# Performance work log

Measured on AMD Instinct MI355X. Metric: run time of the kernel, lower is better.

Reference implementation:

```python
import jax, jax.numpy as jnp
import numpy as np

DIM = 1024
HEADS = 8
HD = DIM // HEADS          # 128
HALF = HD // 2             # 64 complex pairs
EPS = 1e-6
T, L, H, W = 10, 4, 21, 37
TOK_PER_FRAME = 1 + L * (5 + H * W)   # 3129
SK = T * TOK_PER_FRAME                # 31290
SQ = 512
THETA = 10000.0


def _inv_freqs(dim):
    # matches precompute_freqs_cis: 1/theta**(arange(0,dim,2)/dim)
    return 1.0 / THETA ** (np.arange(0, dim, 2)[: dim // 2].astype(np.float64) / dim)


def _angles(t_idx, h_idx, w_idx):
    # 3D RoPE split per precompute_freqs_cis_3d: f gets HD-2*(HD//3)=44 dims, h/w get HD//3=42 each
    hd3 = HD // 3
    inv_f = _inv_freqs(HD - 2 * hd3)  # 22 freqs
    inv_h = _inv_freqs(hd3)           # 21 freqs
    inv_w = _inv_freqs(hd3)           # 21 freqs
    ang = np.concatenate([
        t_idx[:, None] * inv_f[None, :],
        h_idx[:, None] * inv_h[None, :],
        w_idx[:, None] * inv_w[None, :],
    ], axis=-1)  # [S, 64]
    return ang


def _memory_positions():
    # per-frame layout from build_3d_freqs_unified: 1 pose token (h=w=0),
    # then per layer: 5 register tokens (h=w=0) + H*W grid tokens
    h_f, w_f = [0], [0]
    grid_h, grid_w = np.meshgrid(np.arange(H), np.arange(W), indexing='ij')
    for _ in range(L):
        h_f += [0] * 5 + list(grid_h.ravel())
        w_f += [0] * 5 + list(grid_w.ravel())
    h_f = np.asarray(h_f, np.float64)
    w_f = np.asarray(w_f, np.float64)
    t_idx = np.repeat(np.arange(T, dtype=np.float64), TOK_PER_FRAME)
    return t_idx, np.tile(h_f, T), np.tile(w_f, T)


def setup_inputs() -> dict:
    key = jax.random.key(0)
    ks = jax.random.split(key, 8)
    # RoPE angle tables
    tq = np.zeros(SQ)  # use_time_encoding=False for queries -> t=0
    hq = (np.arange(SQ) // W) % H
    wq = np.arange(SQ) % W
    ang_q = _angles(tq.astype(np.float64), hq.astype(np.float64), wq.astype(np.float64))
    tk, hk, wk = _memory_positions()
    ang_k = _angles(tk, hk, wk)
    s = 0.02
    inp = {
        'x': jax.random.normal(ks[0], (1, SQ, DIM), jnp.float32),
        'mem': jax.random.normal(ks[1], (1, SK, DIM), jnp.float32),
        'mask': jax.random.randint(ks[2], (1, SK), 0, 2) > 0,
        'cos_q': jnp.asarray(np.cos(ang_q), jnp.float32),
        'sin_q': jnp.asarray(np.sin(ang_q), jnp.float32),
        'cos_k': jnp.asarray(np.cos(ang_k), jnp.float32),
        'sin_k': jnp.asarray(np.sin(ang_k), jnp.float32),
        'Wq': jax.random.normal(ks[3], (DIM, DIM), jnp.float32) * s,
        'bq': jnp.zeros((DIM,), jnp.float32),
        'Wk': jax.random.normal(ks[4], (DIM, DIM), jnp.float32) * s,
        'bk': jnp.zeros((DIM,), jnp.float32),
        'Wv': jax.random.normal(ks[5], (DIM, DIM), jnp.float32) * s,
        'bv': jnp.zeros((DIM,), jnp.float32),
        'Wo': jax.random.normal(ks[6], (DIM, DIM), jnp.float32) * s,
        'bo': jnp.zeros((DIM,), jnp.float32),
        'gq': jnp.ones((DIM,), jnp.float32),
        'gk': jnp.ones((DIM,), jnp.float32),
    }
    return inp


def _rmsnorm(x, g):
    xf = x.astype(jnp.float32)
    y = xf * jax.lax.rsqrt(jnp.mean(xf * xf, axis=-1, keepdims=True) + EPS)
    return y.astype(x.dtype) * g


def _rope(x, cos, sin):
    # x: [B,S,D]; complex rotation on interleaved pairs per head, freqs shared across heads
    B, S, _ = x.shape
    xh = x.reshape(B, S, HEADS, HALF, 2)
    xr, xi = xh[..., 0], xh[..., 1]
    c = cos[None, :, None, :]
    s = sin[None, :, None, :]
    orr = xr * c - xi * s
    oi = xr * s + xi * c
    return jnp.stack([orr, oi], axis=-1).reshape(B, S, HEADS * HD)


def reference(x, mem, mask, cos_q, sin_q, cos_k, sin_k,
              Wq, bq, Wk, bk, Wv, bv, Wo, bo, gq, gk):
    q = _rmsnorm(x @ Wq.T + bq, gq)
    k = _rmsnorm(mem @ Wk.T + bk, gk)
    v = mem @ Wv.T + bv
    q = _rope(q, cos_q, sin_q)
    k = _rope(k, cos_k, sin_k)
    B, Sq, _ = q.shape
    Sk = k.shape[1]
    qh = q.reshape(B, Sq, HEADS, HD)
    kh = k.reshape(B, Sk, HEADS, HD)
    vh = v.reshape(B, Sk, HEADS, HD)
    scores = jnp.einsum('bqnd,bknd->bnqk', qh, kh) / jnp.sqrt(jnp.float32(HD))
    bias = jnp.where(mask[:, None, None, :], 0.0, -jnp.inf).astype(scores.dtype)
    attn = jax.nn.softmax(scores + bias, axis=-1)
    out = jnp.einsum('bnqk,bknd->bqnd', attn, vh).reshape(B, Sq, DIM)
    return out @ Wo.T + bo
```

## Files before the change

### kernel.cpp

```cpp
#include <hip/hip_runtime.h>
#include <cstdint>

typedef __bf16 bf16;
typedef __bf16 bf16x8 __attribute__((ext_vector_type(8)));
typedef __bf16 bf16x4 __attribute__((ext_vector_type(4)));
typedef float f32x4 __attribute__((ext_vector_type(4)));

#define DEVINL __device__ __forceinline__

namespace {
constexpr int DIM = 1024, HEADS = 8, HD = 128, HALF = 64;
constexpr int SQ = 512;
constexpr int SK = 31290;
constexpr int SKP = 31488;
constexpr int NSPLIT = 24;

constexpr long OFF_MEMB = 0;
constexpr long OFF_XB   = OFF_MEMB + (long)SKP * DIM * 2;
constexpr long OFF_WKV  = OFF_XB + (long)SQ * DIM * 2;
constexpr long OFF_WQ   = OFF_WKV + 2048L * DIM * 2;
constexpr long OFF_WO   = OFF_WQ + (long)DIM * DIM * 2;
constexpr long OFF_BKV  = OFF_WO + (long)DIM * DIM * 2;
constexpr long OFF_KPRE = OFF_BKV + 2048L * 4;
constexpr long OFF_VT   = OFF_KPRE + (long)SKP * DIM * 2;
constexpr long OFF_QPRE = OFF_VT + (long)DIM * SKP * 2;
constexpr long OFF_QR   = OFF_QPRE + (long)SQ * DIM * 4;
constexpr long OFF_BIAS = OFF_QR + (long)SQ * DIM * 2;
constexpr long OFF_ML   = OFF_BIAS + (long)SKP * 4;
constexpr long OFF_AO   = OFF_ML + (long)NSPLIT * HEADS * SQ * 2 * 4;
constexpr long OFF_IDX  = OFF_AO + (long)SQ * DIM * 2;
constexpr long OFF_NKC  = OFF_IDX + 31744L * 4;
constexpr long OFF_OP   = OFF_MEMB;
}

DEVINL void gl_lds16(const void* g, void* l) {
  __builtin_amdgcn_global_load_lds(
      (__attribute__((address_space(1))) void*)(void*)g,
      (__attribute__((address_space(3))) void*)l, 16, 0, 0);
}


__global__ __launch_bounds__(1024) void k_scan(const int* __restrict__ mask,
                                               int* __restrict__ idx,
                                               int* __restrict__ nkcp) {
  int tid = threadIdx.x, lane = tid & 63, wv = tid >> 6;
  __shared__ int wsum[16];
  __shared__ int base;
  if (tid == 0) base = 0;
  __syncthreads();
  for (int c = 0; c < 31; ++c) {
    int i = c * 1024 + tid;
    int m = (i < SK) ? (mask[i] != 0) : 0;
    int v = m;
    #pragma unroll
    for (int off = 1; off < 64; off <<= 1) {
      int t = __shfl_up(v, off);
      if (lane >= off) v += t;
    }
    if (lane == 63) wsum[wv] = v;
    __syncthreads();
    int woff = 0;
    for (int j = 0; j < wv; ++j) woff += wsum[j];
    if (m) idx[base + woff + v - 1] = i;
    __syncthreads();
    if (tid == 0) {
      int tot = 0;
      for (int j = 0; j < 16; ++j) tot += wsum[j];
      base += tot;
    }
    __syncthreads();
  }
  if (tid == 0) *nkcp = base;
}


__global__ __launch_bounds__(256) void k_cvt_mem(const float* __restrict__ mem,
                                                 const int* __restrict__ idx,
                                                 const int* __restrict__ nkcp,
                                                 bf16* __restrict__ memb) {
  long i = (long)blockIdx.x * 256 + threadIdx.x;
  long e = i * 8;
  if (e >= (long)SKP * DIM) return;
  int row = (int)(e >> 10);
  int nkc = *nkcp;
  int lim = ((((nkc + 63) & ~63) + 255) & ~255);
  if (row >= lim) return;
  bf16x8 o;
  if (row < nkc) {
    long se = ((long)idx[row] << 10) + (e & 1023);
    float4 a = *(const float4*)(mem + se);
    float4 b = *(const float4*)(mem + se + 4);
    o[0] = (bf16)a.x; o[1] = (bf16)a.y; o[2] = (bf16)a.z; o[3] = (bf16)a.w;
    o[4] = (bf16)b.x; o[5] = (bf16)b.y; o[6] = (bf16)b.z; o[7] = (bf16)b.w;
  } else {
    #pragma unroll
    for (int j = 0; j < 8; ++j) o[j] = (bf16)0.0f;
  }
  *(bf16x8*)(memb + e) = o;
}

__global__ __launch_bounds__(256) void k_cvt(const float* __restrict__ s,
                                             bf16* __restrict__ d, long n8) {
  long i = (long)blockIdx.x * 256 + threadIdx.x;
  if (i >= n8) return;
  long e = i * 8;
  float4 a = *(const float4*)(s + e);
  float4 b = *(const float4*)(s + e + 4);
  bf16x8 o;
  o[0] = (bf16)a.x; o[1] = (bf16)a.y; o[2] = (bf16)a.z; o[3] = (bf16)a.w;
  o[4] = (bf16)b.x; o[5] = (bf16)b.y; o[6] = (bf16)b.z; o[7] = (bf16)b.w;
  *(bf16x8*)(d + e) = o;
}

__global__ __launch_bounds__(256) void k_build_wkv(const float* __restrict__ Wk,
    const float* __restrict__ Wv, const float* __restrict__ bk,
    const float* __restrict__ bv, bf16* __restrict__ WB, float* __restrict__ bKV) {
  long i = (long)blockIdx.x * 256 + threadIdx.x;
  long e = i * 8;
  if (e < 2048L * 1024) {
    int n = (int)(e >> 10);
    const float* src = (n < 1024) ? (Wk + e) : (Wv + e - 1024L * 1024);
    float4 a = *(const float4*)(src);
    float4 b = *(const float4*)(src + 4);
    bf16x8 o;
    o[0] = (bf16)a.x; o[1] = (bf16)a.y; o[2] = (bf16)a.z; o[3] = (bf16)a.w;
    o[4] = (bf16)b.x; o[5] = (bf16)b.y; o[6] = (bf16)b.z; o[7] = (bf16)b.w;
    *(bf16x8*)(WB + e) = o;
  }
  if (i < 2048) bKV[i] = (i < 1024) ? bk[i] : bv[i - 1024];
}

__global__ __launch_bounds__(256) void k_bias(const int* __restrict__ nkcp,
                                              float* __restrict__ biasA) {
  int k = blockIdx.x * 256 + threadIdx.x;
  if (k < SKP) biasA[k] = (k < *nkcp) ? 0.0f : -1e30f;
}


template<int MODE>
__global__ __launch_bounds__(256, 2)
void k_gemm(const bf16* __restrict__ A, const bf16* __restrict__ B,
            const float* __restrict__ bias, int Mtiles, int Ntiles,
            float* __restrict__ outF, int ldF,
            bf16* __restrict__ outK, bf16* __restrict__ outVT) {
  constexpr int K = 1024;
  __shared__ char lds[32768];
  char* ldsA = lds;
  char* ldsB = lds + 16384;
  int tid = threadIdx.x;
  int w = tid >> 6, lane = tid & 63;
  int cpx = gridDim.x >> 3;
  int bid = (blockIdx.x & 7) * cpx + (blockIdx.x >> 3);
  int mt = bid / Ntiles, nt = bid % Ntiles;
  int m0 = mt * 128, n0 = nt * 128;
  int wm = w >> 1, wn = w & 1;
  int cl = lane & 15, rg = lane >> 4;

  f32x4 acc[4][4] = {};

  int rowi = lane >> 3, g = lane & 7;
  for (int kt = 0; kt < K / 64; ++kt) {
    #pragma unroll
    for (int j = 0; j < 4; ++j) {
      int rb = (w * 4 + j) * 8;
      int row = rb + rowi;
      int gs = g ^ (row & 7);
      gl_lds16((const char*)(A + (long)(m0 + row) * K + kt * 64) + gs * 16, ldsA + rb * 128);
      gl_lds16((const char*)(B + (long)(n0 + row) * K + kt * 64) + gs * 16, ldsB + rb * 128);
    }
    __syncthreads();
    #pragma unroll
    for (int ks = 0; ks < 2; ++ks) {
      bf16x8 af[4], bfr[4];
      #pragma unroll
      for (int i = 0; i < 4; ++i) {
        int rowA = wm * 64 + i * 16 + cl;
        int c = ks * 4 + rg;
        af[i] = *(const bf16x8*)(ldsA + rowA * 128 + ((c ^ (rowA & 7)) * 16));
        int rowB = wn * 64 + i * 16 + cl;
        bfr[i] = *(const bf16x8*)(ldsB + rowB * 128 + ((c ^ (rowB & 7)) * 16));
      }
      #pragma unroll
      for (int mf = 0; mf < 4; ++mf)
        #pragma unroll
        for (int nf = 0; nf < 4; ++nf)
          acc[mf][nf] = __builtin_amdgcn_mfma_f32_16x16x32_bf16(af[mf], bfr[nf], acc[mf][nf], 0, 0, 0);
    }
    __syncthreads();
  }

  #pragma unroll
  for (int mf = 0; mf < 4; ++mf) {
    #pragma unroll
    for (int nf = 0; nf < 4; ++nf) {
      int n = n0 + wn * 64 + nf * 16 + cl;
      float bval = bias[n];
      int mb = m0 + wm * 64 + mf * 16 + rg * 4;
      #pragma unroll
      for (int rr = 0; rr < 4; ++rr)
        outF[(long)(mb + rr) * ldF + n] = acc[mf][nf][rr] + bval;
    }
  }
}


#define KV_PHASE(P)                                                                   \
  {                                                                                   \
    bf16x8 a00 = dsA(cur, 2 * (P), 0),     a01 = dsA(cur, 2 * (P), 1);                \
    bf16x8 a10 = dsA(cur, 2 * (P) + 1, 0), a11 = dsA(cur, 2 * (P) + 1, 1);            \
    __builtin_amdgcn_s_setprio(1);                                                    \
    _Pragma("unroll")                                                                 \
    for (int nf = 0; nf < 4; ++nf) {                                                  \
      acc[2 * (P)][nf]     = __builtin_amdgcn_mfma_f32_16x16x32_bf16(a00, bb[nf][0], acc[2 * (P)][nf], 0, 0, 0);     \
      acc[2 * (P) + 1][nf] = __builtin_amdgcn_mfma_f32_16x16x32_bf16(a10, bb[nf][0], acc[2 * (P) + 1][nf], 0, 0, 0); \
    }                                                                                 \
    _Pragma("unroll")                                                                 \
    for (int nf = 0; nf < 4; ++nf) {                                                  \
      acc[2 * (P)][nf]     = __builtin_amdgcn_mfma_f32_16x16x32_bf16(a01, bb[nf][1], acc[2 * (P)][nf], 0, 0, 0);     \
      acc[2 * (P) + 1][nf] = __builtin_amdgcn_mfma_f32_16x16x32_bf16(a11, bb[nf][1], acc[2 * (P) + 1][nf], 0, 0, 0); \
    }                                                                                 \
    __builtin_amdgcn_s_setprio(0);                                                    \
  }

__global__ __launch_bounds__(512)
void k_gemm_kv(const bf16* __restrict__ A, const bf16* __restrict__ B,
               const float* __restrict__ bias, const int* __restrict__ nkcp,
               bf16* __restrict__ outK, bf16* __restrict__ outVT) {
  constexpr int K = 1024, NTK = 16;
  __shared__ char lds[131072];
  const int tid = threadIdx.x;
  const int w = tid >> 6, lane = tid & 63;
  const int mt = blockIdx.x >> 3, nt = blockIdx.x & 7;
  const int m0 = mt * 256, n0 = nt * 256;
  if (m0 >= ((*nkcp + 63) & ~63)) return;
  const int wm = w >> 2, wn = w & 3;
  const int cl = lane & 15, rg = lane >> 4;
  const int srow = lane >> 3, sg = lane & 7;

  f32x4 acc[8][4] = {};

  auto stage = [&](int b, int kt, int isB, int cr) {
    const bf16* src = isB ? B : A;
    int r = cr + w * 8 + srow;
    int gs = sg ^ (r & 7);
    const char* gp = (const char*)(src + (long)((isB ? n0 : m0) + r) * K + kt * 64) + gs * 16;
    char* lp = lds + b * 65536 + isB * 32768 + (cr + w * 8) * 128;
    gl_lds16(gp, lp);
  };
  auto dsA = [&](int b, int mf, int ks) -> bf16x8 {
    int r = wm * 128 + mf * 16 + cl;
    int c = ks * 4 + rg;
    return *(const bf16x8*)(lds + b * 65536 + r * 128 + ((c ^ (r & 7)) * 16));
  };
  auto dsB = [&](int b, int nf, int ks) -> bf16x8 {
    int r = wn * 64 + nf * 16 + cl;
    int c = ks * 4 + rg;
    return *(const bf16x8*)(lds + b * 65536 + 32768 + r * 128 + ((c ^ (r & 7)) * 16));
  };

  stage(0, 0, 1, 0);   stage(0, 0, 1, 64);
  stage(0, 0, 1, 128); stage(0, 0, 1, 192);
  stage(0, 0, 0, 0);   stage(0, 0, 0, 128);
  stage(0, 0, 0, 64);  stage(0, 0, 0, 192);

  for (int t = 0; t < NTK; ++t) {
    const int cur = t & 1, nxt = cur ^ 1;
    const bool pre = (t + 1 < NTK);
    bf16x8 bb[4][2];

    if (pre) {
      stage(nxt, t + 1, 1, 0); stage(nxt, t + 1, 1, 64);
      asm volatile("s_waitcnt vmcnt(4)\ns_barrier" ::: "memory");
    } else {
      asm volatile("s_waitcnt vmcnt(2)\ns_barrier" ::: "memory");
    }
    #pragma unroll
    for (int nf = 0; nf < 4; ++nf) { bb[nf][0] = dsB(cur, nf, 0); bb[nf][1] = dsB(cur, nf, 1); }
    KV_PHASE(0)
    if (pre) { stage(nxt, t + 1, 1, 128); stage(nxt, t + 1, 1, 192); }
    KV_PHASE(1)
    if (pre) {
      stage(nxt, t + 1, 0, 0); stage(nxt, t + 1, 0, 128);
      asm volatile("s_waitcnt vmcnt(6)\ns_barrier" ::: "memory");
    } else {
      asm volatile("s_waitcnt vmcnt(0)\ns_barrier" ::: "memory");
    }
    KV_PHASE(2)
    if (pre) { stage(nxt, t + 1, 0, 64); stage(nxt, t + 1, 0, 192); }
    KV_PHASE(3)
    asm volatile("s_barrier" ::: "memory");
  }

  if (nt < 4) {
    #pragma unroll
    for (int mf = 0; mf < 8; ++mf)
      #pragma unroll
      for (int nf = 0; nf < 4; ++nf) {
        int n = n0 + wn * 64 + nf * 16 + cl;
        float bval = bias[n];
        int mrow = m0 + wm * 128 + mf * 16 + rg * 4;
        #pragma unroll
        for (int rr = 0; rr < 4; ++rr)
          outK[(long)(mrow + rr) * 1024 + n] = (bf16)(acc[mf][nf][rr] + bval);
      }
  } else {
    #pragma unroll
    for (int mf = 0; mf < 8; ++mf)
      #pragma unroll
      for (int nf = 0; nf < 4; ++nf) {
        int n = n0 + wn * 64 + nf * 16 + cl;
        float bval = bias[n];
        int mrow = m0 + wm * 128 + mf * 16 + rg * 4;
        bf16x4 pk;
        #pragma unroll
        for (int rr = 0; rr < 4; ++rr) pk[rr] = (bf16)(acc[mf][nf][rr] + bval);
        *(bf16x4*)(outVT + (long)(n - 1024) * SKP + mrow) = pk;
      }
  }
}


__global__ __launch_bounds__(256) void k_fuse_q(const float* __restrict__ QP,
    bf16* __restrict__ Qr, const float* __restrict__ gg,
    const float* __restrict__ cosT, const float* __restrict__ sinT) {
  int row = blockIdx.x, tid = threadIdx.x;
  int d0 = tid * 4;
  float4 t = *(const float4*)(QP + (long)row * DIM + d0);
  float v0 = t.x, v1 = t.y, v2 = t.z, v3 = t.w;
  float ss = v0 * v0 + v1 * v1 + v2 * v2 + v3 * v3;
  #pragma unroll
  for (int m = 1; m < 64; m <<= 1) ss += __shfl_xor(ss, m);
  __shared__ float red[4];
  if ((tid & 63) == 0) red[tid >> 6] = ss;
  __syncthreads();
  float rn = rsqrtf((red[0] + red[1] + red[2] + red[3]) * (1.0f / DIM) + 1e-6f);
  v0 *= rn * gg[d0]; v1 *= rn * gg[d0 + 1]; v2 *= rn * gg[d0 + 2]; v3 *= rn * gg[d0 + 3];
  int i0 = (d0 & 127) >> 1;
  float c0 = cosT[(long)row * HALF + i0], s0 = sinT[(long)row * HALF + i0];
  float c1 = cosT[(long)row * HALF + i0 + 1], s1 = sinT[(long)row * HALF + i0 + 1];
  bf16x4 o = { (bf16)(v0 * c0 - v1 * s0), (bf16)(v0 * s0 + v1 * c0),
               (bf16)(v2 * c1 - v3 * s1), (bf16)(v2 * s1 + v3 * c1) };
  *(bf16x4*)(Qr + (long)row * DIM + d0) = o;
}

__global__ __launch_bounds__(256) void k_fuse_k(bf16* __restrict__ KP,
    const float* __restrict__ gg, const float* __restrict__ cosT,
    const float* __restrict__ sinT, const int* __restrict__ idx,
    const int* __restrict__ nkcp) {
  int row = blockIdx.x, tid = threadIdx.x;
  int nkc = *nkcp;
  if (row >= ((nkc + 63) & ~63)) return;
  int orig = (row < nkc) ? idx[row] : 0;
  int d0 = tid * 4;
  bf16x4 t = *(const bf16x4*)(KP + (long)row * DIM + d0);
  float v0 = (float)t[0], v1 = (float)t[1], v2 = (float)t[2], v3 = (float)t[3];
  float ss = v0 * v0 + v1 * v1 + v2 * v2 + v3 * v3;
  #pragma unroll
  for (int m = 1; m < 64; m <<= 1) ss += __shfl_xor(ss, m);
  __shared__ float red[4];
  if ((tid & 63) == 0) red[tid >> 6] = ss;
  __syncthreads();
  float rn = rsqrtf((red[0] + red[1] + red[2] + red[3]) * (1.0f / DIM) + 1e-6f);
  v0 *= rn * gg[d0]; v1 *= rn * gg[d0 + 1]; v2 *= rn * gg[d0 + 2]; v3 *= rn * gg[d0 + 3];
  int i0 = (d0 & 127) >> 1;
  float c0 = cosT[(long)orig * HALF + i0], s0 = sinT[(long)orig * HALF + i0];
  float c1 = cosT[(long)orig * HALF + i0 + 1], s1 = sinT[(long)orig * HALF + i0 + 1];
  bf16x4 o = { (bf16)(v0 * c0 - v1 * s0), (bf16)(v0 * s0 + v1 * c0),
               (bf16)(v2 * c1 - v3 * s1), (bf16)(v2 * s1 + v3 * c1) };
  *(bf16x4*)(KP + (long)row * DIM + d0) = o;
}


__global__ __launch_bounds__(256, 2)
void k_attn(const bf16* __restrict__ Kr, const bf16* __restrict__ VT,
            const bf16* __restrict__ Qr, const float* __restrict__ biasA,
            const int* __restrict__ nkcp,
            float* __restrict__ Opart, float* __restrict__ ml) {
  __shared__ char lds[49152];
  char* ldsK = lds;
  char* ldsV = lds + 16384;
  int tid = threadIdx.x, w = tid >> 6, lane = tid & 63;
  char* ldsP = lds + 32768 + w * 4096;
  int bid = blockIdx.x;
  int swz = (bid & 7) * 96 + (bid >> 3);
  int sp = swz >> 5, h = (swz >> 2) & 7, qb = swz & 3;
  int NTC = (*nkcp + 63) >> 6;
  int t0 = (sp * NTC) / NSPLIT;
  int t1 = ((sp + 1) * NTC) / NSPLIT;
  int cl = lane & 15, rg = lane >> 4;
  int qbase = qb * 128 + w * 32;

  bf16x8 qf[2][4];
  #pragma unroll
  for (int mf = 0; mf < 2; ++mf)
    #pragma unroll
    for (int ks = 0; ks < 4; ++ks)
      qf[mf][ks] = *(const bf16x8*)(Qr + (long)(qbase + mf * 16 + cl) * DIM + h * HD + ks * 32 + rg * 8);

  bf16x8 ones;
  #pragma unroll
  for (int j = 0; j < 8; ++j) ones[j] = (bf16)1.0f;

  f32x4 Oa[2][8] = {};
  f32x4 l_acc[2] = {};
  float m_r[2] = {-1e30f, -1e30f};

  const float sc = 0.08838834764831845f;
  for (int t = t0; t < t1; ++t) {
    int k0 = t * 64;
    __syncthreads();
    {
      int rK = lane >> 4, gK = lane & 15;
      #pragma unroll
      for (int j = 0; j < 4; ++j) {
        int rb = w * 16 + j * 4;
        int row = rb + rK;
        int gs = gK ^ (row & 7);
        gl_lds16((const char*)(Kr + (long)(k0 + row) * DIM + h * HD) + gs * 16,
                 ldsK + rb * 256);
      }
      int rV = lane >> 3, gV = lane & 7;
      #pragma unroll
      for (int j = 0; j < 4; ++j) {
        int db = w * 32 + j * 8;
        int d = db + rV;
        int gs = gV ^ (d & 7);
        gl_lds16((const char*)(VT + (long)(h * HD + d) * SKP + k0) + gs * 16,
                 ldsV + db * 128);
      }
    }
    __syncthreads();

    f32x4 sa[2][4] = {};
    #pragma unroll
    for (int ks = 0; ks < 4; ++ks) {
      #pragma unroll
      for (int nf = 0; nf < 4; ++nf) {
        int key = nf * 16 + cl;
        int c = ks * 4 + rg;
        bf16x8 kb = *(const bf16x8*)(ldsK + key * 256 + ((c ^ (key & 7)) * 16));
        sa[0][nf] = __builtin_amdgcn_mfma_f32_16x16x32_bf16(qf[0][ks], kb, sa[0][nf], 0, 0, 0);
        sa[1][nf] = __builtin_amdgcn_mfma_f32_16x16x32_bf16(qf[1][ks], kb, sa[1][nf], 0, 0, 0);
      }
    }

    float bia[4];
    #pragma unroll
    for (int nf = 0; nf < 4; ++nf) bia[nf] = biasA[k0 + nf * 16 + cl];

    #pragma unroll
    for (int mf = 0; mf < 2; ++mf) {
      char* ldsPmf = ldsP + mf * 2048;
      #pragma unroll
      for (int nf = 0; nf < 4; ++nf)
        #pragma unroll
        for (int r = 0; r < 4; ++r) sa[mf][nf][r] = sa[mf][nf][r] * sc + bia[nf];
      float mx = sa[mf][0][0];
      #pragma unroll
      for (int nf = 0; nf < 4; ++nf)
        #pragma unroll
        for (int r = 0; r < 4; ++r) mx = fmaxf(mx, sa[mf][nf][r]);
      mx = fmaxf(mx, __shfl_xor(mx, 1));
      mx = fmaxf(mx, __shfl_xor(mx, 2));
      mx = fmaxf(mx, __shfl_xor(mx, 4));
      mx = fmaxf(mx, __shfl_xor(mx, 8));
      bool grew = mx > m_r[mf] + 6.0f;
      if (__any(grew)) {
        float mn = grew ? mx : m_r[mf];
        float scale = __expf(m_r[mf] - mn);
        m_r[mf] = mn;
        l_acc[mf] *= scale;
        #pragma unroll
        for (int df = 0; df < 8; ++df) Oa[mf][df] *= scale;
      }
      #pragma unroll
      for (int nf = 0; nf < 4; ++nf)
        #pragma unroll
        for (int r = 0; r < 4; ++r) {
          float p = __expf(sa[mf][nf][r] - m_r[mf]);
          int qr = rg * 4 + r;
          int col = nf * 16 + cl;
          int gp = (col >> 3) ^ (qr & 7);
          *(bf16*)(ldsPmf + qr * 128 + gp * 16 + (col & 7) * 2) = (bf16)p;
        }
    }

    #pragma unroll
    for (int ks = 0; ks < 2; ++ks) {
      int c = ks * 4 + rg;
      bf16x8 pa0 = *(const bf16x8*)(ldsP + cl * 128 + ((c ^ (cl & 7)) * 16));
      bf16x8 pa1 = *(const bf16x8*)(ldsP + 2048 + cl * 128 + ((c ^ (cl & 7)) * 16));
      l_acc[0] = __builtin_amdgcn_mfma_f32_16x16x32_bf16(pa0, ones, l_acc[0], 0, 0, 0);
      l_acc[1] = __builtin_amdgcn_mfma_f32_16x16x32_bf16(pa1, ones, l_acc[1], 0, 0, 0);
      #pragma unroll
      for (int df = 0; df < 8; ++df) {
        int d = df * 16 + cl;
        bf16x8 vb = *(const bf16x8*)(ldsV + d * 128 + ((c ^ (d & 7)) * 16));
        Oa[0][df] = __builtin_amdgcn_mfma_f32_16x16x32_bf16(pa0, vb, Oa[0][df], 0, 0, 0);
        Oa[1][df] = __builtin_amdgcn_mfma_f32_16x16x32_bf16(pa1, vb, Oa[1][df], 0, 0, 0);
      }
    }
  }

  long rowb = (long)(sp * HEADS + h) * SQ + qbase;
  #pragma unroll
  for (int mf = 0; mf < 2; ++mf) {
    #pragma unroll
    for (int df = 0; df < 8; ++df)
      #pragma unroll
      for (int r = 0; r < 4; ++r) {
        int qr = mf * 16 + rg * 4 + r;
        Opart[(rowb + qr) * HD + df * 16 + cl] = Oa[mf][df][r];
      }
    if (cl == 0) {
      #pragma unroll
      for (int r = 0; r < 4; ++r) {
        int qr = mf * 16 + rg * 4 + r;
        ml[(rowb + qr) * 2] = m_r[mf];
        ml[(rowb + qr) * 2 + 1] = l_acc[mf][r];
      }
    }
  }
}

__global__ __launch_bounds__(128) void k_combine(const float* __restrict__ Opart,
    const float* __restrict__ ml, bf16* __restrict__ AO) {
  int bid = blockIdx.x;
  int h = bid >> 9, qq = bid & 511;
  int d = threadIdx.x;
  float M = -1e30f;
  #pragma unroll 4
  for (int s2 = 0; s2 < NSPLIT; ++s2) {
    long mi = (long)(s2 * HEADS + h) * SQ + qq;
    M = fmaxf(M, ml[mi * 2]);
  }
  float L = 0.f, acc = 0.f;
  #pragma unroll 4
  for (int s2 = 0; s2 < NSPLIT; ++s2) {
    long mi = (long)(s2 * HEADS + h) * SQ + qq;
    float wgt = __expf(ml[mi * 2] - M);
    L += wgt * ml[mi * 2 + 1];
    acc += wgt * Opart[mi * HD + d];
  }
  AO[(long)qq * DIM + h * HD + d] = (bf16)(acc / L);
}


extern "C" void kernel_launch(void* const* d_in, const int* in_sizes, int n_in,
                              void* d_out, int out_size, void* d_ws, size_t ws_size,
                              hipStream_t stream) {
  const float* x     = (const float*)d_in[0];
  const float* mem   = (const float*)d_in[1];
  const int*   mask  = (const int*)d_in[2];
  const float* cos_q = (const float*)d_in[3];
  const float* sin_q = (const float*)d_in[4];
  const float* cos_k = (const float*)d_in[5];
  const float* sin_k = (const float*)d_in[6];
  const float* Wq    = (const float*)d_in[7];
  const float* bq    = (const float*)d_in[8];
  const float* Wk    = (const float*)d_in[9];
  const float* bk    = (const float*)d_in[10];
  const float* Wv    = (const float*)d_in[11];
  const float* bv    = (const float*)d_in[12];
  const float* Wo    = (const float*)d_in[13];
  const float* bo    = (const float*)d_in[14];
  const float* gq    = (const float*)d_in[15];
  const float* gk    = (const float*)d_in[16];

  char* ws = (char*)d_ws;
  bf16*  memb = (bf16*)(ws + OFF_MEMB);
  bf16*  xb   = (bf16*)(ws + OFF_XB);
  bf16*  WkvB = (bf16*)(ws + OFF_WKV);
  bf16*  WqB  = (bf16*)(ws + OFF_WQ);
  bf16*  WoB  = (bf16*)(ws + OFF_WO);
  float* bKV  = (float*)(ws + OFF_BKV);
  bf16*  Kpre = (bf16*)(ws + OFF_KPRE);
  bf16*  VT   = (bf16*)(ws + OFF_VT);
  float* Qpre = (float*)(ws + OFF_QPRE);
  bf16*  Qr   = (bf16*)(ws + OFF_QR);
  float* biasA= (float*)(ws + OFF_BIAS);
  float* Opart= (float*)(ws + OFF_OP);
  float* mlb  = (float*)(ws + OFF_ML);
  bf16*  AO   = (bf16*)(ws + OFF_AO);
  int*   idx  = (int*)(ws + OFF_IDX);
  int*   nkcp = (int*)(ws + OFF_NKC);

  k_scan<<<dim3(1), dim3(1024), 0, stream>>>(mask, idx, nkcp);
  k_cvt_mem<<<dim3(SKP * DIM / 8 / 256), dim3(256), 0, stream>>>(mem, idx, nkcp, memb);
  k_cvt<<<dim3(SQ * DIM / 8 / 256), dim3(256), 0, stream>>>(x, xb, (long)(SQ * DIM / 8));
  k_cvt<<<dim3(DIM * DIM / 8 / 256), dim3(256), 0, stream>>>(Wq, WqB, (long)(DIM * DIM / 8));
  k_cvt<<<dim3(DIM * DIM / 8 / 256), dim3(256), 0, stream>>>(Wo, WoB, (long)(DIM * DIM / 8));
  k_build_wkv<<<dim3(2048 * DIM / 8 / 256), dim3(256), 0, stream>>>(Wk, Wv, bk, bv, WkvB, bKV);
  k_bias<<<dim3(SKP / 256), dim3(256), 0, stream>>>(nkcp, biasA);

  k_gemm<0><<<dim3(4 * 8), dim3(256), 0, stream>>>(xb, WqB, bq, 4, 8, Qpre, DIM,
                                                   (bf16*)nullptr, (bf16*)nullptr);
  k_gemm_kv<<<dim3(984), dim3(512), 0, stream>>>(memb, WkvB, bKV, nkcp, Kpre, VT);

  k_fuse_q<<<dim3(SQ), dim3(256), 0, stream>>>(Qpre, Qr, gq, cos_q, sin_q);
  k_fuse_k<<<dim3(SKP), dim3(256), 0, stream>>>(Kpre, gk, cos_k, sin_k, idx, nkcp);

  k_attn<<<dim3(NSPLIT * HEADS * 4), dim3(256), 0, stream>>>(Kpre, VT, Qr, biasA, nkcp, Opart, mlb);
  k_combine<<<dim3(HEADS * SQ), dim3(128), 0, stream>>>(Opart, mlb, AO);

  k_gemm<0><<<dim3(4 * 8), dim3(256), 0, stream>>>(AO, WoB, bo, 4, 8, (float*)d_out, DIM,
                                                   (bf16*)nullptr, (bf16*)nullptr);
  (void)in_sizes; (void)n_in; (void)out_size; (void)ws_size;
}
```

Measured before the change: 278.9 us.

## Merge conversion kernels, fuse bias fill, ballot-based scan, add KV gemm barriers

Replaces the shuffle-based prefix scan with a ballot/popcount compaction and folds the attention bias fill into the memory conversion kernel. The separate x, Wq, Wo and Wk/Wv conversion launches are merged into a single prep kernel to cut launch overhead. Extra workgroup barriers are inserted between phases of the KV GEMM main loop, likely to guard LDS buffer reuse, at the cost of more synchronization.

```diff
diff --git a/kernel.cpp b/kernel.cpp
--- a/kernel.cpp
+++ b/kernel.cpp
@@ -51,20 +51,18 @@
   for (int c = 0; c < 31; ++c) {
     int i = c * 1024 + tid;
     int m = (i < SK) ? (mask[i] != 0) : 0;
-    int v = m;
-    #pragma unroll
-    for (int off = 1; off < 64; off <<= 1) {
-      int t = __shfl_up(v, off);
-      if (lane >= off) v += t;
-    }
-    if (lane == 63) wsum[wv] = v;
+    unsigned long long bal = __ballot(m);
+    int wpre = (int)__popcll(bal & ((1ull << lane) - 1ull));
+    if (lane == 0) wsum[wv] = (int)__popcll(bal);
     __syncthreads();
     int woff = 0;
-    for (int j = 0; j < wv; ++j) woff += wsum[j];
-    if (m) idx[base + woff + v - 1] = i;
+    #pragma unroll
+    for (int j = 0; j < 16; ++j) woff += (j < wv) ? wsum[j] : 0;
+    if (m) idx[base + woff + wpre] = i;
     __syncthreads();
     if (tid == 0) {
       int tot = 0;
+      #pragma unroll
       for (int j = 0; j < 16; ++j) tot += wsum[j];
       base += tot;
     }
@@ -77,7 +75,8 @@
 __global__ __launch_bounds__(256) void k_cvt_mem(const float* __restrict__ mem,
                                                  const int* __restrict__ idx,
                                                  const int* __restrict__ nkcp,
-                                                 bf16* __restrict__ memb) {
+                                                 bf16* __restrict__ memb,
+                                                 float* __restrict__ biasA) {
   long i = (long)blockIdx.x * 256 + threadIdx.x;
   long e = i * 8;
   if (e >= (long)SKP * DIM) return;
@@ -85,6 +84,7 @@
   int nkc = *nkcp;
   int lim = ((((nkc + 63) & ~63) + 255) & ~255);
   if (row >= lim) return;
+  if ((e & 1023) == 0) biasA[row] = (row < nkc) ? 0.0f : -1e30f;
   bf16x8 o;
   if (row < nkc) {
     long se = ((long)idx[row] << 10) + (e & 1023);
@@ -99,41 +99,41 @@
   *(bf16x8*)(memb + e) = o;
 }
 
-__global__ __launch_bounds__(256) void k_cvt(const float* __restrict__ s,
-                                             bf16* __restrict__ d, long n8) {
+__global__ __launch_bounds__(256) void k_prep(const float* __restrict__ x,
+    const float* __restrict__ Wq, const float* __restrict__ Wo,
+    const float* __restrict__ Wk, const float* __restrict__ Wv,
+    const float* __restrict__ bk, const float* __restrict__ bv,
+    bf16* __restrict__ xb, bf16* __restrict__ WqB, bf16* __restrict__ WoB,
+    bf16* __restrict__ WkvB, float* __restrict__ bKV) {
   long i = (long)blockIdx.x * 256 + threadIdx.x;
-  if (i >= n8) return;
-  long e = i * 8;
-  float4 a = *(const float4*)(s + e);
-  float4 b = *(const float4*)(s + e + 4);
+  constexpr long n_x = 65536, n_w = 131072;
+  const float* src;
+  bf16* dst;
+  long off;
+  if (i < n_x) { src = x; dst = xb; off = i; }
+  else if (i < n_x + n_w) { src = Wq; dst = WqB; off = i - n_x; }
+  else if (i < n_x + 2 * n_w) { src = Wo; dst = WoB; off = i - n_x - n_w; }
+  else if (i < n_x + 2 * n_w + 262144) {
+    long j = i - n_x - 2 * n_w;
+    long e = j * 8;
+    int n = (int)(e >> 10);
+    const float* s2 = (n < 1024) ? (Wk + e) : (Wv + e - 1024L * 1024);
+    float4 a = *(const float4*)(s2);
+    float4 b = *(const float4*)(s2 + 4);
+    bf16x8 o;
+    o[0] = (bf16)a.x; o[1] = (bf16)a.y; o[2] = (bf16)a.z; o[3] = (bf16)a.w;
+    o[4] = (bf16)b.x; o[5] = (bf16)b.y; o[6] = (bf16)b.z; o[7] = (bf16)b.w;
+    *(bf16x8*)(WkvB + e) = o;
+    if (j < 2048) bKV[j] = (j < 1024) ? bk[j] : bv[j - 1024];
+    return;
+  } else return;
+  long e = off * 8;
+  float4 a = *(const float4*)(src + e);
+  float4 b = *(const float4*)(src + e + 4);
   bf16x8 o;
   o[0] = (bf16)a.x; o[1] = (bf16)a.y; o[2] = (bf16)a.z; o[3] = (bf16)a.w;
   o[4] = (bf16)b.x; o[5] = (bf16)b.y; o[6] = (bf16)b.z; o[7] = (bf16)b.w;
-  *(bf16x8*)(d + e) = o;
-}
-
-__global__ __launch_bounds__(256) void k_build_wkv(const float* __restrict__ Wk,
-    const float* __restrict__ Wv, const float* __restrict__ bk,
-    const float* __restrict__ bv, bf16* __restrict__ WB, float* __restrict__ bKV) {
-  long i = (long)blockIdx.x * 256 + threadIdx.x;
-  long e = i * 8;
-  if (e < 2048L * 1024) {
-    int n = (int)(e >> 10);
-    const float* src = (n < 1024) ? (Wk + e) : (Wv + e - 1024L * 1024);
-    float4 a = *(const float4*)(src);
-    float4 b = *(const float4*)(src + 4);
-    bf16x8 o;
-    o[0] = (bf16)a.x; o[1] = (bf16)a.y; o[2] = (bf16)a.z; o[3] = (bf16)a.w;
-    o[4] = (bf16)b.x; o[5] = (bf16)b.y; o[6] = (bf16)b.z; o[7] = (bf16)b.w;
-    *(bf16x8*)(WB + e) = o;
-  }
-  if (i < 2048) bKV[i] = (i < 1024) ? bk[i] : bv[i - 1024];
-}
-
-__global__ __launch_bounds__(256) void k_bias(const int* __restrict__ nkcp,
-                                              float* __restrict__ biasA) {
-  int k = blockIdx.x * 256 + threadIdx.x;
-  if (k < SKP) biasA[k] = (k < *nkcp) ? 0.0f : -1e30f;
+  *(bf16x8*)(dst + e) = o;
 }
 
 
@@ -277,8 +277,10 @@
     #pragma unroll
     for (int nf = 0; nf < 4; ++nf) { bb[nf][0] = dsB(cur, nf, 0); bb[nf][1] = dsB(cur, nf, 1); }
     KV_PHASE(0)
+    asm volatile("s_barrier" ::: "memory");
     if (pre) { stage(nxt, t + 1, 1, 128); stage(nxt, t + 1, 1, 192); }
     KV_PHASE(1)
+    asm volatile("s_barrier" ::: "memory");
     if (pre) {
       stage(nxt, t + 1, 0, 0); stage(nxt, t + 1, 0, 128);
       asm volatile("s_waitcnt vmcnt(6)\ns_barrier" ::: "memory");
@@ -286,6 +288,7 @@
       asm volatile("s_waitcnt vmcnt(0)\ns_barrier" ::: "memory");
     }
     KV_PHASE(2)
+    asm volatile("s_barrier" ::: "memory");
     if (pre) { stage(nxt, t + 1, 0, 64); stage(nxt, t + 1, 0, 192); }
     KV_PHASE(3)
     asm volatile("s_barrier" ::: "memory");
@@ -586,12 +589,9 @@
   int*   nkcp = (int*)(ws + OFF_NKC);
 
   k_scan<<<dim3(1), dim3(1024), 0, stream>>>(mask, idx, nkcp);
-  k_cvt_mem<<<dim3(SKP * DIM / 8 / 256), dim3(256), 0, stream>>>(mem, idx, nkcp, memb);
-  k_cvt<<<dim3(SQ * DIM / 8 / 256), dim3(256), 0, stream>>>(x, xb, (long)(SQ * DIM / 8));
-  k_cvt<<<dim3(DIM * DIM / 8 / 256), dim3(256), 0, stream>>>(Wq, WqB, (long)(DIM * DIM / 8));
-  k_cvt<<<dim3(DIM * DIM / 8 / 256), dim3(256), 0, stream>>>(Wo, WoB, (long)(DIM * DIM / 8));
-  k_build_wkv<<<dim3(2048 * DIM / 8 / 256), dim3(256), 0, stream>>>(Wk, Wv, bk, bv, WkvB, bKV);
-  k_bias<<<dim3(SKP / 256), dim3(256), 0, stream>>>(nkcp, biasA);
+  k_cvt_mem<<<dim3(SKP * DIM / 8 / 256), dim3(256), 0, stream>>>(mem, idx, nkcp, memb, biasA);
+  k_prep<<<dim3(2304), dim3(256), 0, stream>>>(x, Wq, Wo, Wk, Wv, bk, bv,
+                                               xb, WqB, WoB, WkvB, bKV);
 
   k_gemm<0><<<dim3(4 * 8), dim3(256), 0, stream>>>(xb, WqB, bq, 4, 8, Qpre, DIM,
                                                    (bf16*)nullptr, (bf16*)nullptr);
```

Result: faster. 257.1 us (-7.8%).
